# Optimization experiments

Measured on AMD Instinct MI355X. Metric: run time of the kernel, lower is better.

Reference implementation:

```python
import jax, jax.numpy as jnp
import numpy as np

SAMPLE_RATE = 44100
MAX_DURATION = 5.0
IR_LEN = int(SAMPLE_RATE * MAX_DURATION)   # 220500 taps (~5 s reverb tail)
AUDIO_LEN = SAMPLE_RATE * 60               # 60 s of mono audio


def setup_inputs() -> dict:
    key = jax.random.key(0)
    k1, k2 = jax.random.split(key)
    audio = jax.random.normal(k1, (1, AUDIO_LEN), dtype=jnp.float32)
    ir = jax.random.normal(k2, (IR_LEN,), dtype=jnp.float32)  # learned impulse response parameter
    return {"audio": audio, "ir": ir}


def _fft_correlate_valid(audio, ir):
    """Valid cross-correlation of (audio zero-padded by M-1) with ir.

    Matches torch: pad audio with M-1 trailing zeros, then conv1d (which is
    cross-correlation) in 'valid' mode -> output length N. Computed via FFT
    (O(N log N)) instead of direct O(N*M) convolution; identical math up to
    floating-point rounding.
    """
    B, N = audio.shape
    M = ir.shape[0]
    full = (N + M - 1) + M - 1          # full linear conv length of padded signal
    nfft = 1 << int(np.ceil(np.log2(full)))
    # trailing zero-pad covers both the explicit M-1 padding and FFT padding
    x = jnp.pad(audio, ((0, 0), (0, nfft - N)))
    k = jnp.pad(ir[::-1], (0, nfft - M))  # flip kernel: conv(x, flip(ir)) == correlate(x, ir)
    y = jnp.fft.irfft(jnp.fft.rfft(x, axis=-1) * jnp.fft.rfft(k), n=nfft, axis=-1)
    # valid cross-correlation region of the padded signal: indices [M-1, M-1+N)
    return jax.lax.dynamic_slice_in_dim(y, M - 1, N, axis=-1)


def reference(audio, ir):
    y = _fft_correlate_valid(audio, ir)       # [1, N]
    return y / jnp.max(jnp.abs(y))            # global max-abs normalization
```

## Files before the change

kernel.cpp:

```cpp
#include <hip/hip_runtime.h>
#include <hip/hip_fp16.h>


#define L_FFT (1 << 20)
#define GSTRIDE 273
#define PSCALE (1.0f / 1048576.0f)

__device__ __forceinline__ float2 h2f(__half2 h) { return __half22float2(h); }
__device__ __forceinline__ __half2 f2h(float2 v) { return __floats2half2_rn(v.x, v.y); }

__device__ __forceinline__ float2 cmul(float2 a, float2 b) {
    return make_float2(a.x * b.x - a.y * b.y, a.x * b.y + a.y * b.x);
}

__device__ __forceinline__ void rad4(float2 a, float2 b, float2 c, float2 d,
                                     float2& o0, float2& o1, float2& o2, float2& o3) {
    float2 apc = make_float2(a.x + c.x, a.y + c.y);
    float2 amc = make_float2(a.x - c.x, a.y - c.y);
    float2 bpd = make_float2(b.x + d.x, b.y + d.y);
    float2 bmd = make_float2(b.x - d.x, b.y - d.y);
    o0 = make_float2(apc.x + bpd.x, apc.y + bpd.y);
    o2 = make_float2(apc.x - bpd.x, apc.y - bpd.y);
    o1 = make_float2(amc.x + bmd.y, amc.y - bmd.x);
    o3 = make_float2(amc.x - bmd.y, amc.y + bmd.x);
}

__device__ __forceinline__ void dft16(float2 x[16]) {
    float2 tt[16];
    rad4(x[0], x[4], x[8],  x[12], tt[0],  tt[1],  tt[2],  tt[3]);
    rad4(x[1], x[5], x[9],  x[13], tt[4],  tt[5],  tt[6],  tt[7]);
    rad4(x[2], x[6], x[10], x[14], tt[8],  tt[9],  tt[10], tt[11]);
    rad4(x[3], x[7], x[11], x[15], tt[12], tt[13], tt[14], tt[15]);
    const float C1 = 0.92387953251128675613f, S1 = 0.38268343236508977173f;
    const float C2 = 0.70710678118654752440f;
    const float2 W1 = make_float2( C1, -S1);
    const float2 W2 = make_float2( C2, -C2);
    const float2 W3 = make_float2( S1, -C1);
    const float2 W6 = make_float2(-C2, -C2);
    const float2 W9 = make_float2(-C1,  S1);
    tt[5]  = cmul(tt[5],  W1);
    tt[6]  = cmul(tt[6],  W2);
    tt[7]  = cmul(tt[7],  W3);
    tt[9]  = cmul(tt[9],  W2);
    tt[10] = make_float2(tt[10].y, -tt[10].x);
    tt[11] = cmul(tt[11], W6);
    tt[13] = cmul(tt[13], W3);
    tt[14] = cmul(tt[14], W6);
    tt[15] = cmul(tt[15], W9);
    rad4(tt[0], tt[4], tt[8],  tt[12], x[0], x[4], x[8],  x[12]);
    rad4(tt[1], tt[5], tt[9],  tt[13], x[1], x[5], x[9],  x[13]);
    rad4(tt[2], tt[6], tt[10], tt[14], x[2], x[6], x[10], x[14]);
    rad4(tt[3], tt[7], tt[11], tt[15], x[3], x[7], x[11], x[15]);
}

__device__ __forceinline__ void fft256_core(float2 x[16], int i, int gi,
                                            float2* lds) {
    dft16(x);
    float sa, ca;
    __sincosf(-6.28318530717958647692f * (float)i * (1.0f / 256.0f), &sa, &ca);
    float2 w1 = make_float2(ca, sa);
    float2 w = w1;
#pragma unroll
    for (int k1 = 1; k1 < 16; ++k1) {
        x[k1] = cmul(x[k1], w);
        w = cmul(w, w1);
    }
    float2* base = lds + gi * GSTRIDE;
#pragma unroll
    for (int k1 = 0; k1 < 16; ++k1) base[i * 17 + k1] = x[k1];
    __syncthreads();
#pragma unroll
    for (int q1 = 0; q1 < 16; ++q1) x[q1] = base[q1 * 17 + i];
    dft16(x);
}

__device__ __forceinline__ void stage256_store(float2 x[16], __half2* db,
                                               int g, int i, int J, int log2J,
                                               float invLn) {
    int j = g & (J - 1);
    int np = g >> log2J;
    float base = -6.28318530717958647692f * (float)np * invLn;
    float sa, ca;
    __sincosf(base * (float)i, &sa, &ca);
    float2 w = make_float2(ca, sa);
    __sincosf(base * 16.0f, &sa, &ca);
    float2 w16 = make_float2(ca, sa);
    size_t ob = (size_t)256 * (g - j) + j;
#pragma unroll
    for (int k2 = 0; k2 < 16; ++k2) {
        db[ob + (size_t)(i + 16 * k2) * J] = f2h(cmul(x[k2], w));
        w = cmul(w, w16);
    }
}

__device__ __forceinline__ void store_j1_coalesced(float2 x[16], __half2* db,
                                                   int bx, int gi, int i, int tid,
                                                   float2* lds, float invL) {
    int g = bx * 16 + gi;
    float base = -6.28318530717958647692f * (float)g * invL;
    float sa, ca;
    __sincosf(base * (float)i, &sa, &ca);
    float2 w = make_float2(ca, sa);
    __sincosf(base * 16.0f, &sa, &ca);
    float2 w16 = make_float2(ca, sa);
    __syncthreads();
#pragma unroll
    for (int k2 = 0; k2 < 16; ++k2) {
        int e = 256 * gi + i + 16 * k2;
        lds[e + (e >> 8)] = cmul(x[k2], w);
        w = cmul(w, w16);
    }
    __syncthreads();
    __half2* dwin = db + (size_t)4096 * bx;
#pragma unroll
    for (int c = 0; c < 16; ++c) {
        int e2 = tid + 256 * c;
        dwin[e2] = f2h(lds[e2 + (e2 >> 8)]);
    }
}

__global__ void fwd1_pack(const float* __restrict__ audio,
                          const float* __restrict__ ir,
                          __half2* __restrict__ dst, int N, int M, int V) {
    __shared__ float2 lds[16 * GSTRIDE];
    int tid = threadIdx.x;
    int gi = tid & 15, i = tid >> 4;
    int bx = blockIdx.x, slot = blockIdx.y;
    int g = bx * 16 + gi;
    __half2* db = dst + (size_t)slot * L_FFT;

    float2 x[16];
#pragma unroll
    for (int q2 = 0; q2 < 16; ++q2) {
        int idx = g + (i + 16 * q2) * (L_FFT / 256);
        float2 v;
        if (slot == 0) {
            v = make_float2(audio[idx], audio[idx + V]);
        } else if (slot == 1) {
            float a2 = (idx + 2 * V < N) ? audio[idx + 2 * V] : 0.f;
            float a3 = (idx + 3 * V < N) ? audio[idx + 3 * V] : 0.f;
            v = make_float2(a2, a3);
        } else {
            v = make_float2((idx < M) ? ir[idx] : 0.f, 0.f);
        }
        x[q2] = v;
    }
    fft256_core(x, i, gi, lds);
    store_j1_coalesced(x, db, bx, gi, i, tid, lds, 1.0f / (float)L_FFT);
}

__global__ void inv1(const __half2* __restrict__ src, __half2* __restrict__ dst) {
    __shared__ float2 lds[16 * GSTRIDE];
    int tid = threadIdx.x;
    int gi = tid & 15, i = tid >> 4;
    int bx = blockIdx.x;
    int g = bx * 16 + gi;
    size_t boff = (size_t)blockIdx.y * L_FFT;
    const __half2* sb = src + boff;
    __half2* db = dst + boff;
    float2 x[16];
#pragma unroll
    for (int q2 = 0; q2 < 16; ++q2)
        x[q2] = h2f(sb[g + (i + 16 * q2) * (L_FFT / 256)]);
    fft256_core(x, i, gi, lds);
    store_j1_coalesced(x, db, bx, gi, i, tid, lds, 1.0f / (float)L_FFT);
}

__global__ void stage256(const __half2* __restrict__ src, __half2* __restrict__ dst,
                         int J, int log2J, float invLn) {
    __shared__ float2 lds[16 * GSTRIDE];
    int tid = threadIdx.x;
    int gi = tid & 15, i = tid >> 4;
    int g = blockIdx.x * 16 + gi;
    size_t boff = (size_t)blockIdx.y * L_FFT;
    const __half2* sb = src + boff;
    __half2* db = dst + boff;
    float2 x[16];
#pragma unroll
    for (int q2 = 0; q2 < 16; ++q2)
        x[q2] = h2f(sb[g + (i + 16 * q2) * (L_FFT / 256)]);
    fft256_core(x, i, gi, lds);
    stage256_store(x, db, g, i, J, log2J, invLn);
}

__global__ void fwd3_spectral(const __half2* __restrict__ A,
                              __half2* __restrict__ B) {
    __shared__ float2 XS[256 * 17];
    int tid = threadIdx.x;
    int isFwd = (tid < 128);
    int j = isFwd ? tid : (tid - 128);
    int gf = blockIdx.x * 128 + j;
    int g = isFwd ? gf : ((65536 - gf) & 65535);
    int ptid = isFwd ? (tid + 128) : (tid - 128);

    float2 h[16];
#pragma unroll
    for (int q = 0; q < 16; ++q)
        h[q] = h2f(A[(size_t)2 * L_FFT + g + (size_t)q * 65536]);
    dft16(h);
#pragma unroll
    for (int p = 0; p < 2; ++p) {
        float2 x[16];
#pragma unroll
        for (int q = 0; q < 16; ++q)
            x[q] = h2f(A[(size_t)p * L_FFT + g + (size_t)q * 65536]);
        dft16(x);
        __syncthreads();
#pragma unroll
        for (int r = 0; r < 16; ++r) XS[tid * 17 + r] = x[r];
        __syncthreads();
#pragma unroll
        for (int r = 0; r < 16; ++r) {
            int mi = (g == 0) ? ((16 - r) & 15) : (15 - r);
            float2 Z  = x[r];
            float2 Zr = XS[ptid * 17 + mi];
            float2 H  = h[r];
            float2 X0 = make_float2(0.5f * (Z.x + Zr.x), 0.5f * (Z.y - Zr.y));
            float2 X1 = make_float2(0.5f * (Z.y + Zr.y), 0.5f * (Zr.x - Z.x));
            float2 G0 = make_float2(X0.x * H.x + X0.y * H.y, X0.y * H.x - X0.x * H.y);
            float2 G1 = make_float2(X1.x * H.x + X1.y * H.y, X1.y * H.x - X1.x * H.y);
            B[(size_t)p * L_FFT + g + (size_t)r * 65536] =
                f2h(make_float2((G0.x - G1.y) * PSCALE,
                                -(G0.y + G1.x) * PSCALE));
        }
    }
}

__global__ void inv3_out(const __half2* __restrict__ src, float* __restrict__ out,
                         float* __restrict__ partials, int N, int V) {
    int g = blockIdx.x * blockDim.x + threadIdx.x;
    int p = blockIdx.y;
    const __half2* sb = src + (size_t)p * L_FFT;
    float2 x[16];
#pragma unroll
    for (int q = 0; q < 16; ++q) x[q] = h2f(sb[g + q * 65536]);
    dft16(x);
    int se = 2 * p, so = 2 * p + 1;
    int lenO = (p == 1) ? (N - 3 * V) : V;
    float m = 0.f;
#pragma unroll
    for (int r = 0; r < 16; ++r) {
        int n = g + r * 65536;
        float vr = x[r].x, vi = -x[r].y;
        if (n < V)    { out[(size_t)se * V + n] = vr; m = fmaxf(m, fabsf(vr)); }
        if (n < lenO) { out[(size_t)so * V + n] = vi; m = fmaxf(m, fabsf(vi)); }
    }
    for (int o = 32; o > 0; o >>= 1) m = fmaxf(m, __shfl_xor(m, o));
    __shared__ float sm[4];
    int lane = threadIdx.x & 63, wv = threadIdx.x >> 6;
    if (lane == 0) sm[wv] = m;
    __syncthreads();
    if (threadIdx.x == 0)
        partials[blockIdx.y * gridDim.x + blockIdx.x] =
            fmaxf(fmaxf(sm[0], sm[1]), fmaxf(sm[2], sm[3]));
}

__global__ void norm_fused(float* __restrict__ out,
                           const float* __restrict__ partials, int N) {
    float m = 0.f;
    for (int i = threadIdx.x; i < 512; i += 256) m = fmaxf(m, partials[i]);
    for (int o = 32; o > 0; o >>= 1) m = fmaxf(m, __shfl_xor(m, o));
    __shared__ float sm[4];
    int lane = threadIdx.x & 63, wv = threadIdx.x >> 6;
    if (lane == 0) sm[wv] = m;
    __syncthreads();
    float inv = 1.0f / fmaxf(fmaxf(sm[0], sm[1]), fmaxf(sm[2], sm[3]));
    int stride = gridDim.x * blockDim.x;
    for (int t = blockIdx.x * blockDim.x + threadIdx.x; t < N; t += stride)
        out[t] *= inv;
}

extern "C" void kernel_launch(void* const* d_in, const int* in_sizes, int n_in,
                              void* d_out, int out_size, void* d_ws, size_t ws_size,
                              hipStream_t stream) {
    const float* audio = (const float*)d_in[0];
    const float* ir    = (const float*)d_in[1];
    float* out = (float*)d_out;

    const int N = in_sizes[0];
    const int M = in_sizes[1];
    const int V = L_FFT - M + 1;

    __half2* A = (__half2*)d_ws;
    __half2* B = A + (size_t)3 * L_FFT;
    float* partials = (float*)(B + (size_t)3 * L_FFT);

    const float invLn2 = 1.0f / 4096.0f;

    fwd1_pack<<<dim3(256, 3), 256, 0, stream>>>(audio, ir, B, N, M, V);
    stage256<<<dim3(256, 3), 256, 0, stream>>>(B, A, 256, 8, invLn2);
    fwd3_spectral<<<257, 256, 0, stream>>>(A, B);
    inv1<<<dim3(256, 2), 256, 0, stream>>>(B, A);
    stage256<<<dim3(256, 2), 256, 0, stream>>>(A, B, 256, 8, invLn2);
    inv3_out<<<dim3(256, 2), 256, 0, stream>>>(B, out, partials, N, V);
    norm_fused<<<1024, 256, 0, stream>>>(out, partials, N);
}
```

Measured before the change: 125.7 us.

## Fuse final inverse FFT stage with max-abs normalization via grid-wide atomic barrier

```diff
diff --git a/kernel.cpp b/kernel.cpp
--- a/kernel.cpp
+++ b/kernel.cpp
@@ -226,48 +226,75 @@
     }
 }
 
-__global__ void inv3_out(const __half2* __restrict__ src, float* __restrict__ out,
-                         float* __restrict__ partials, int N, int V) {
-    int g = blockIdx.x * blockDim.x + threadIdx.x;
+__global__ __launch_bounds__(256) void inv3_norm(
+    const __half2* __restrict__ src, float* __restrict__ out,
+    float* __restrict__ partials, unsigned* __restrict__ sync, int N, int V) {
+    __shared__ float sm[4];
+    __shared__ int isLast;
+    __shared__ float invBC;
+    int tid = threadIdx.x;
+    int unit = blockIdx.y * gridDim.x + blockIdx.x;
+    int g = blockIdx.x * 256 + tid;
     int p = blockIdx.y;
     const __half2* sb = src + (size_t)p * L_FFT;
     float2 x[16];
 #pragma unroll
     for (int q = 0; q < 16; ++q) x[q] = h2f(sb[g + q * 65536]);
     dft16(x);
-    int se = 2 * p, so = 2 * p + 1;
     int lenO = (p == 1) ? (N - 3 * V) : V;
     float m = 0.f;
 #pragma unroll
     for (int r = 0; r < 16; ++r) {
         int n = g + r * 65536;
-        float vr = x[r].x, vi = -x[r].y;
-        if (n < V)    { out[(size_t)se * V + n] = vr; m = fmaxf(m, fabsf(vr)); }
-        if (n < lenO) { out[(size_t)so * V + n] = vi; m = fmaxf(m, fabsf(vi)); }
+        if (n < V)    m = fmaxf(m, fabsf(x[r].x));
+        if (n < lenO) m = fmaxf(m, fabsf(x[r].y));
     }
     for (int o = 32; o > 0; o >>= 1) m = fmaxf(m, __shfl_xor(m, o));
-    __shared__ float sm[4];
-    int lane = threadIdx.x & 63, wv = threadIdx.x >> 6;
+    int lane = tid & 63, wv = tid >> 6;
     if (lane == 0) sm[wv] = m;
     __syncthreads();
-    if (threadIdx.x == 0)
-        partials[blockIdx.y * gridDim.x + blockIdx.x] =
-            fmaxf(fmaxf(sm[0], sm[1]), fmaxf(sm[2], sm[3]));
-}
-
-__global__ void norm_fused(float* __restrict__ out,
-                           const float* __restrict__ partials, int N) {
-    float m = 0.f;
-    for (int i = threadIdx.x; i < 512; i += 256) m = fmaxf(m, partials[i]);
-    for (int o = 32; o > 0; o >>= 1) m = fmaxf(m, __shfl_xor(m, o));
-    __shared__ float sm[4];
-    int lane = threadIdx.x & 63, wv = threadIdx.x >> 6;
-    if (lane == 0) sm[wv] = m;
-    __syncthreads();
-    float inv = 1.0f / fmaxf(fmaxf(sm[0], sm[1]), fmaxf(sm[2], sm[3]));
-    int stride = gridDim.x * blockDim.x;
-    for (int t = blockIdx.x * blockDim.x + threadIdx.x; t < N; t += stride)
-        out[t] *= inv;
+    if (tid == 0) {
+        float bm = fmaxf(fmaxf(sm[0], sm[1]), fmaxf(sm[2], sm[3]));
+        __hip_atomic_store(&partials[unit], bm, __ATOMIC_RELAXED,
+                           __HIP_MEMORY_SCOPE_AGENT);
+        __threadfence();
+        unsigned done = atomicAdd(&sync[0], 1u);
+        isLast = (done == 511u) ? 1 : 0;
+    }
+    __syncthreads();
+    if (isLast) {
+        __threadfence();
+        float mm = 0.f;
+        for (int i2 = tid; i2 < 512; i2 += 256)
+            mm = fmaxf(mm, __hip_atomic_load(&partials[i2], __ATOMIC_RELAXED,
+                                             __HIP_MEMORY_SCOPE_AGENT));
+        for (int o = 32; o > 0; o >>= 1) mm = fmaxf(mm, __shfl_xor(mm, o));
+        if (lane == 0) sm[wv] = mm;
+        __syncthreads();
+        if (tid == 0) {
+            float inv = 1.0f / fmaxf(fmaxf(sm[0], sm[1]), fmaxf(sm[2], sm[3]));
+            __hip_atomic_store((float*)&sync[2], inv, __ATOMIC_RELAXED,
+                               __HIP_MEMORY_SCOPE_AGENT);
+            __hip_atomic_store(&sync[1], 1u, __ATOMIC_RELEASE,
+                               __HIP_MEMORY_SCOPE_AGENT);
+        }
+    }
+    if (tid == 0) {
+        while (__hip_atomic_load(&sync[1], __ATOMIC_ACQUIRE,
+                                 __HIP_MEMORY_SCOPE_AGENT) == 0u)
+            __builtin_amdgcn_s_sleep(16);
+        invBC = __hip_atomic_load((float*)&sync[2], __ATOMIC_RELAXED,
+                                  __HIP_MEMORY_SCOPE_AGENT);
+    }
+    __syncthreads();
+    float inv = invBC;
+    int se = 2 * p, so = 2 * p + 1;
+#pragma unroll
+    for (int r = 0; r < 16; ++r) {
+        int n = g + r * 65536;
+        if (n < V)    out[(size_t)se * V + n] = x[r].x * inv;
+        if (n < lenO) out[(size_t)so * V + n] = -x[r].y * inv;
+    }
 }
 
 extern "C" void kernel_launch(void* const* d_in, const int* in_sizes, int n_in,
@@ -284,6 +311,9 @@
     __half2* A = (__half2*)d_ws;
     __half2* B = A + (size_t)3 * L_FFT;
     float* partials = (float*)(B + (size_t)3 * L_FFT);
+    unsigned* syncc = (unsigned*)(partials + 512);
+
+    hipMemsetAsync(syncc, 0, 3 * sizeof(unsigned), stream);
 
     const float invLn2 = 1.0f / 4096.0f;
 
@@ -292,6 +322,5 @@
     fwd3_spectral<<<257, 256, 0, stream>>>(A, B);
     inv1<<<dim3(256, 2), 256, 0, stream>>>(B, A);
     stage256<<<dim3(256, 2), 256, 0, stream>>>(A, B, 256, 8, invLn2);
-    inv3_out<<<dim3(256, 2), 256, 0, stream>>>(B, out, partials, N, V);
-    norm_fused<<<1024, 256, 0, stream>>>(out, partials, N);
-}
+    inv3_norm<<<dim3(256, 2), 256, 0, stream>>>(B, out, partials, syncc, N, V);
+}
```

Result: slower. 163.3 us (+29.9%).
